# Kernel optimization log

Hardware: AMD Instinct MI355X
Metric: run time of the kernel (lower is better)

## Reference

```python
import jax, jax.numpy as jnp
import numpy as np

N = 50000      # nodes
E = 800000     # edges (avg degree 16)
D_IN = 128
D_H = 128
D_OUT = 8


def setup_inputs() -> dict:
    key = jax.random.key(0)
    ks = jax.random.split(key, 12)
    def lin(k, fan_in, shape):
        return (jax.random.normal(k, shape, jnp.float32) / np.float32(np.sqrt(fan_in)))
    return {
        "node_features": jax.random.normal(ks[0], (N, D_IN), jnp.float32),
        "edge_index": jax.random.randint(ks[1], (2, E), 0, N, jnp.int32),
        # 3 GCNConv layers: weight [in, out] + bias [out]
        "W0": lin(ks[2], D_IN, (D_IN, D_H)), "b0": jnp.zeros((D_H,), jnp.float32),
        "W1": lin(ks[3], D_H, (D_H, D_H)),  "b1": jnp.zeros((D_H,), jnp.float32),
        "W2": lin(ks[4], D_H, (D_H, D_H)),  "b2": jnp.zeros((D_H,), jnp.float32),
        # classifier MLP: hidden -> hidden//2 -> output
        "cW1": lin(ks[5], D_H, (D_H, D_H // 2)), "cb1": jnp.zeros((D_H // 2,), jnp.float32),
        "cW2": lin(ks[6], D_H // 2, (D_H // 2, D_OUT)), "cb2": jnp.zeros((D_OUT,), jnp.float32),
    }


def _gcn_norm(edge_index, n):
    # PyG GCNConv default: add self-loops, symmetric D^-1/2 (A+I) D^-1/2 normalization
    loops = jnp.arange(n, dtype=edge_index.dtype)
    src = jnp.concatenate([edge_index[0], loops])   # message sources j
    dst = jnp.concatenate([edge_index[1], loops])   # aggregation targets i
    deg = jax.ops.segment_sum(jnp.ones_like(src, dtype=jnp.float32), dst, num_segments=n)
    dinv = jax.lax.rsqrt(jnp.maximum(deg, 1.0))     # deg >= 1 due to self-loops
    norm = dinv[src] * dinv[dst]                    # [E+N]
    return src, dst, norm


def _gcn_conv(x, W, b, src, dst, norm, n):
    h = x @ W                                        # [N, out] dense transform first (PyG order)
    msg = h[src] * norm[:, None]                     # gather + scale  [E+N, out]
    out = jax.ops.segment_sum(msg, dst, num_segments=n)  # scatter-add
    return out + b


def reference(node_features, edge_index, W0, b0, W1, b1, W2, b2, cW1, cb1, cW2, cb2):
    n = node_features.shape[0]
    src, dst, norm = _gcn_norm(edge_index, n)
    x = jax.nn.relu(_gcn_conv(node_features, W0, b0, src, dst, norm, n))  # dropout is identity in eval
    x = jax.nn.relu(_gcn_conv(x, W1, b1, src, dst, norm, n))
    x = _gcn_conv(x, W2, b2, src, dst, norm, n)       # last conv: no relu/dropout
    # classifier MLP (dropout identity in eval)
    h = jax.nn.relu(x @ cW1 + cb1)
    return h @ cW2 + cb2                              # [N, D_OUT]
```

## Files before the change

kernel.cpp:

```cpp
#include <hip/hip_runtime.h>
#include <hip/hip_fp16.h>


#define CAP 48
#define FPG 512

using half8v  = __attribute__((ext_vector_type(8))) _Float16;
using float4v = __attribute__((ext_vector_type(4))) float;

__global__ __launch_bounds__(256) void fill_kernel(const int* __restrict__ src,
                                                   const int* __restrict__ dst, int e, int n,
                                                   const float* __restrict__ W0,
                                                   const float* __restrict__ W1,
                                                   const float* __restrict__ W2,
                                                   const float* __restrict__ cW1,
                                                   const float* __restrict__ cb1,
                                                   const float* __restrict__ b2,
                                                   int* __restrict__ cnt,
                                                   unsigned short* __restrict__ col,
                                                   __half* __restrict__ Wf0,
                                                   __half* __restrict__ Wf1,
                                                   __half* __restrict__ Wfc,
                                                   float* __restrict__ bc) {
    int b = blockIdx.x;
    int tid = threadIdx.x;
    const int FILLB = 4 * FPG;
    if (b < FILLB) {
        int g = b & 3;
        int cb = b >> 2;
        int npp = (n + 3) >> 2;
        int lo = g * npp;
        int hi = min(lo + npp, n);
        int step = FPG * 256;
        int base = cb * 256 + tid;
        int dv[7], sv[7];
        #pragma unroll
        for (int k = 0; k < 7; k++) {
            int i = base + k * step;
            if (i < e) {
                dv[k] = __builtin_nontemporal_load(dst + i);
                sv[k] = __builtin_nontemporal_load(src + i);
            }
        }
        #pragma unroll
        for (int k = 0; k < 7; k++) {
            int i = base + k * step;
            if (i < e) {
                int d = dv[k];
                if (d >= lo && d < hi) {
                    int c = atomicAdd(&cnt[d], 1);
                    if (c < CAP) col[d * CAP + c] = (unsigned short)sv[k];
                }
            }
        }
        return;
    }
    b -= FILLB;
    if (b < 16) {
        int t = b * 256 + tid;
        const float* W = (t < 2048) ? W0 : W1;
        __half* Wf = (t < 2048) ? Wf0 : Wf1;
        int u = t & 2047;
        int lane = u & 63, tile = (u >> 6) & 7, kk = u >> 9;
        int k0 = kk * 32 + (lane >> 4) * 8;
        int nn = tile * 16 + (lane & 15);
        __half tmp[8];
        #pragma unroll
        for (int j = 0; j < 8; j++) tmp[j] = __float2half(W[(k0 + j) * 128 + nn]);
        *(float4*)(Wf + (size_t)u * 8) = *(const float4*)tmp;
        return;
    }
    b -= 16;
    if (b < 4) {
        int u = b * 256 + tid;
        int lane = u & 63, tile = (u >> 6) & 3, kk = u >> 8;
        int k0 = kk * 32 + (lane >> 4) * 8;
        int nn = tile * 16 + (lane & 15);
        float a[8] = {};
        for (int m = 0; m < 128; m++) {
            float c = cW1[m * 64 + nn];
            #pragma unroll
            for (int j = 0; j < 8; j++) a[j] = fmaf(W2[(k0 + j) * 128 + m], c, a[j]);
        }
        __half tmp[8];
        #pragma unroll
        for (int j = 0; j < 8; j++) tmp[j] = __float2half(a[j]);
        *(float4*)(Wfc + (size_t)u * 8) = *(const float4*)tmp;
        return;
    }
    if (tid < 64) {
        float a = cb1[tid];
        for (int k = 0; k < 128; k++) a = fmaf(b2[k], cW1[k * 64 + tid], a);
        bc[tid] = a;
    }
}

__global__ __launch_bounds__(256) void gemm0_mfma(const float* __restrict__ x,
                                                  const __half* __restrict__ Wf,
                                                  const int* __restrict__ cnt,
                                                  __half* __restrict__ out, int n) {
    int tid = threadIdx.x;
    int wv = tid >> 6, lane = tid & 63;
    int row0 = blockIdx.x * 64 + wv * 16;
    int m = lane & 15, q = lane >> 4;
    int ra = min(row0 + m, n - 1);
    const float* xrow = x + (size_t)ra * 128 + q * 8;
    const _Float16* wf = (const _Float16*)Wf + (size_t)lane * 8;
    float4v acc[8] = {};
    #pragma unroll
    for (int kk = 0; kk < 4; kk++) {
        float4 xa = *(const float4*)(xrow + kk * 32);
        float4 xb = *(const float4*)(xrow + kk * 32 + 4);
        half8v a;
        a[0] = (_Float16)xa.x; a[1] = (_Float16)xa.y;
        a[2] = (_Float16)xa.z; a[3] = (_Float16)xa.w;
        a[4] = (_Float16)xb.x; a[5] = (_Float16)xb.y;
        a[6] = (_Float16)xb.z; a[7] = (_Float16)xb.w;
        #pragma unroll
        for (int t8 = 0; t8 < 8; t8++) {
            half8v bfr = *(const half8v*)(wf + (size_t)(kk * 8 + t8) * 512);
            acc[t8] = __builtin_amdgcn_mfma_f32_16x16x32_f16(a, bfr, acc[t8], 0, 0, 0);
        }
    }
    int rowv[4];
    float dr[4];
    #pragma unroll
    for (int r = 0; r < 4; r++) {
        rowv[r] = row0 + q * 4 + r;
        dr[r] = (rowv[r] < n) ? rsqrtf((float)(cnt[rowv[r]] + 1)) : 0.f;
    }
    #pragma unroll
    for (int t8 = 0; t8 < 8; t8++) {
        #pragma unroll
        for (int r = 0; r < 4; r++) {
            if (rowv[r] < n)
                out[(size_t)(t8 >> 1) * n * 32 + (size_t)rowv[r] * 32 + (t8 & 1) * 16 + m] =
                    __float2half(acc[t8][r] * dr[r]);
        }
    }
}

__global__ __launch_bounds__(256) void gemm_mfma(const __half* __restrict__ x,
                                                 const __half* __restrict__ Wf,
                                                 const int* __restrict__ cnt,
                                                 __half* __restrict__ out, int n) {
    int tid = threadIdx.x;
    int wv = tid >> 6, lane = tid & 63;
    int row0 = blockIdx.x * 64 + wv * 16;
    int m = lane & 15, q = lane >> 4;
    int ra = min(row0 + m, n - 1);
    const _Float16* xb = (const _Float16*)x;
    const _Float16* wf = (const _Float16*)Wf + (size_t)lane * 8;
    float4v acc[8] = {};
    #pragma unroll
    for (int kk = 0; kk < 4; kk++) {
        int tki = kk * 2 + (q >> 1);
        half8v a = *(const half8v*)(xb + (size_t)(tki >> 1) * n * 32 + (size_t)ra * 32 +
                                    (tki & 1) * 16 + (q & 1) * 8);
        #pragma unroll
        for (int t8 = 0; t8 < 8; t8++) {
            half8v bfr = *(const half8v*)(wf + (size_t)(kk * 8 + t8) * 512);
            acc[t8] = __builtin_amdgcn_mfma_f32_16x16x32_f16(a, bfr, acc[t8], 0, 0, 0);
        }
    }
    int rowv[4];
    float dr[4];
    #pragma unroll
    for (int r = 0; r < 4; r++) {
        rowv[r] = row0 + q * 4 + r;
        dr[r] = (rowv[r] < n) ? rsqrtf((float)(cnt[rowv[r]] + 1)) : 0.f;
    }
    #pragma unroll
    for (int t8 = 0; t8 < 8; t8++) {
        #pragma unroll
        for (int r = 0; r < 4; r++) {
            if (rowv[r] < n)
                out[(size_t)(t8 >> 1) * n * 32 + (size_t)rowv[r] * 32 + (t8 & 1) * 16 + m] =
                    __float2half(acc[t8][r] * dr[r]);
        }
    }
}

__global__ __launch_bounds__(256) void gemm_t_mfma(const __half* __restrict__ x,
                                                   const __half* __restrict__ Wf,
                                                   __half* __restrict__ out, int n) {
    int tid = threadIdx.x;
    int wv = tid >> 6, lane = tid & 63;
    int row0 = blockIdx.x * 64 + wv * 16;
    int m = lane & 15, q = lane >> 4;
    int ra = min(row0 + m, n - 1);
    const _Float16* xb = (const _Float16*)x;
    const _Float16* wf = (const _Float16*)Wf + (size_t)lane * 8;
    float4v acc[4] = {};
    #pragma unroll
    for (int kk = 0; kk < 4; kk++) {
        int tki = kk * 2 + (q >> 1);
        half8v a = *(const half8v*)(xb + (size_t)(tki >> 1) * n * 32 + (size_t)ra * 32 +
                                    (tki & 1) * 16 + (q & 1) * 8);
        #pragma unroll
        for (int t8 = 0; t8 < 4; t8++) {
            half8v bfr = *(const half8v*)(wf + (size_t)(kk * 4 + t8) * 512);
            acc[t8] = __builtin_amdgcn_mfma_f32_16x16x32_f16(a, bfr, acc[t8], 0, 0, 0);
        }
    }
    int rowv[4];
    #pragma unroll
    for (int r = 0; r < 4; r++) rowv[r] = row0 + q * 4 + r;
    #pragma unroll
    for (int t8 = 0; t8 < 4; t8++) {
        #pragma unroll
        for (int r = 0; r < 4; r++) {
            if (rowv[r] < n)
                out[(size_t)(t8 >> 1) * n * 32 + (size_t)rowv[r] * 32 + (t8 & 1) * 16 + m] =
                    __float2half(acc[t8][r]);
        }
    }
}

__global__ __launch_bounds__(256) void agg_tiled(const __half* __restrict__ hin,
                                                 const int* __restrict__ cnt,
                                                 const unsigned short* __restrict__ col,
                                                 const float* __restrict__ bias,
                                                 __half* __restrict__ hout,
                                                 int n, float one, int relu,
                                                 int scale_out, int ftsh) {
    int ft = blockIdx.x & ((1 << ftsh) - 1);
    int nb = blockIdx.x >> ftsh;
    int tid = threadIdx.x;
    int node = nb * 64 + (tid >> 2);
    int q = tid & 3;
    int ic = min(node, n - 1);
    const _Float16* hsl = (const _Float16*)hin + (size_t)ft * n * 32 + q * 8;
    int ci = cnt[ic];
    int len = min(ci, CAP);
    float di = rsqrtf((float)(ci + 1));
    half8v s = *(const half8v*)(hsl + (size_t)ic * 32);
    float acc[8];
    #pragma unroll
    for (int t = 0; t < 8; t++) acc[t] = (float)s[t];
    const unsigned short* crow = col + ic * CAP;
    int nfull = len >> 4;
    for (int f = 0; f < nfull; f++) {
        int k0 = f * 16;
        uint4 ca = *(const uint4*)(crow + k0);
        uint4 cb = *(const uint4*)(crow + k0 + 8);
        int j[16];
        j[0]  = ca.x & 0xffff; j[1]  = ca.x >> 16;
        j[2]  = ca.y & 0xffff; j[3]  = ca.y >> 16;
        j[4]  = ca.z & 0xffff; j[5]  = ca.z >> 16;
        j[6]  = ca.w & 0xffff; j[7]  = ca.w >> 16;
        j[8]  = cb.x & 0xffff; j[9]  = cb.x >> 16;
        j[10] = cb.y & 0xffff; j[11] = cb.y >> 16;
        j[12] = cb.z & 0xffff; j[13] = cb.z >> 16;
        j[14] = cb.w & 0xffff; j[15] = cb.w >> 16;
        half8v v[16];
        #pragma unroll
        for (int u = 0; u < 16; u++) v[u] = *(const half8v*)(hsl + (size_t)j[u] * 32);
        #pragma unroll
        for (int u = 0; u < 16; u++) {
            #pragma unroll
            for (int t = 0; t < 8; t++) acc[t] = fmaf((float)v[u][t], one, acc[t]);
        }
    }
    int k0 = nfull * 16;
    if (k0 < len) {
        int rem = len - k0;
        uint4 ca = *(const uint4*)(crow + k0);
        uint4 cb = *(const uint4*)(crow + k0 + 8);
        int j[16];
        j[0]  = ca.x & 0xffff; j[1]  = ca.x >> 16;
        j[2]  = ca.y & 0xffff; j[3]  = ca.y >> 16;
        j[4]  = ca.z & 0xffff; j[5]  = ca.z >> 16;
        j[6]  = ca.w & 0xffff; j[7]  = ca.w >> 16;
        j[8]  = cb.x & 0xffff; j[9]  = cb.x >> 16;
        j[10] = cb.y & 0xffff; j[11] = cb.y >> 16;
        j[12] = cb.z & 0xffff; j[13] = cb.z >> 16;
        j[14] = cb.w & 0xffff; j[15] = cb.w >> 16;
        float w[16];
        half8v v[16];
        #pragma unroll
        for (int u = 0; u < 16; u++) {
            bool val = u < rem;
            w[u] = val ? one : 0.f;
            int jj = val ? j[u] : ic;
            v[u] = *(const half8v*)(hsl + (size_t)jj * 32);
        }
        #pragma unroll
        for (int u = 0; u < 16; u++) {
            #pragma unroll
            for (int t = 0; t < 8; t++) acc[t] = fmaf((float)v[u][t], w[u], acc[t]);
        }
    }
    if (node < n) {
        float post = scale_out ? di : 1.f;
        half8v o;
        #pragma unroll
        for (int t = 0; t < 8; t++) {
            float bv = bias ? bias[ft * 32 + q * 8 + t] : 0.f;
            float a = fmaf(acc[t], di, bv);
            if (relu) a = fmaxf(a, 0.f);
            o[t] = (_Float16)(a * post);
        }
        *(half8v*)((_Float16*)hout + (size_t)ft * n * 32 + (size_t)node * 32 + q * 8) = o;
    }
}

__global__ __launch_bounds__(256) void cls_kernel(const __half* __restrict__ h,
                                                  const float* __restrict__ cW2,
                                                  const float* __restrict__ cb2,
                                                  float* __restrict__ out, int n) {
    __shared__ _Float16 hs[64][72];
    int tid = threadIdx.x;
    int node0 = blockIdx.x * 64;
    int nl = tid >> 2, q = tid & 3;
    int ic = min(node0 + nl, n - 1);
    #pragma unroll
    for (int ft = 0; ft < 2; ft++) {
        half8v v = *(const half8v*)((const _Float16*)h + (size_t)ft * n * 32 +
                                    (size_t)ic * 32 + q * 8);
        *(half8v*)&hs[nl][ft * 32 + q * 8] = v;
    }
    __syncthreads();
    #pragma unroll
    for (int p = 0; p < 2; p++) {
        int idx = p * 256 + tid;
        int rl = idx >> 3, c2 = idx & 7;
        int row = node0 + rl;
        if (row < n) {
            float a = cb2[c2];
            #pragma unroll 8
            for (int k = 0; k < 64; k++) a = fmaf((float)hs[rl][k], cW2[k * 8 + c2], a);
            out[row * 8 + c2] = a;
        }
    }
}

extern "C" void kernel_launch(void* const* d_in, const int* in_sizes, int n_in,
                              void* d_out, int out_size, void* d_ws, size_t ws_size,
                              hipStream_t stream) {
    const float* x   = (const float*)d_in[0];
    const int*   ei  = (const int*)d_in[1];
    const float* W0  = (const float*)d_in[2];
    const float* b0  = (const float*)d_in[3];
    const float* W1  = (const float*)d_in[4];
    const float* b1  = (const float*)d_in[5];
    const float* W2  = (const float*)d_in[6];
    const float* b2  = (const float*)d_in[7];
    const float* cW1 = (const float*)d_in[8];
    const float* cb1 = (const float*)d_in[9];
    const float* cW2 = (const float*)d_in[10];
    const float* cb2 = (const float*)d_in[11];
    float* out = (float*)d_out;

    int N = in_sizes[0] / 128;
    int E = in_sizes[1] / 2;
    const int* src = ei;
    const int* dst = ei + E;

    char* ws = (char*)d_ws;
    size_t off = 0;
    auto alloc = [&](size_t bytes) {
        void* p = ws + off;
        off = (off + bytes + 255) & ~(size_t)255;
        return p;
    };
    int* cnt              = (int*)alloc((size_t)N * 4);
    unsigned short* col   = (unsigned short*)alloc((size_t)N * CAP * 2);
    __half* Wf0           = (__half*)alloc((size_t)128 * 128 * 2);
    __half* Wf1           = (__half*)alloc((size_t)128 * 128 * 2);
    __half* Wfc           = (__half*)alloc((size_t)128 * 64 * 2);
    float* bc             = (float*)alloc(64 * 4);
    __half* hA            = (__half*)alloc((size_t)N * 128 * 2);
    __half* hB            = (__half*)alloc((size_t)N * 128 * 2);

    hipMemsetAsync(cnt, 0, (size_t)N * 4, stream);

    fill_kernel<<<4 * FPG + 21, 256, 0, stream>>>(src, dst, E, N, W0, W1, W2,
                                                  cW1, cb1, b2,
                                                  cnt, col, Wf0, Wf1, Wfc, bc);

    int NBLK = (N + 63) / 64;
    gemm0_mfma<<<NBLK, 256, 0, stream>>>(x, Wf0, cnt, hA, N);
    agg_tiled<<<NBLK * 4, 256, 0, stream>>>(hA, cnt, col, b0, hB, N, 1.0f, 1, 0, 2);
    gemm_mfma<<<NBLK, 256, 0, stream>>>(hB, Wf1, cnt, hA, N);
    agg_tiled<<<NBLK * 4, 256, 0, stream>>>(hA, cnt, col, b1, hB, N, 1.0f, 1, 1, 2);
    gemm_t_mfma<<<NBLK, 256, 0, stream>>>(hB, Wfc, hA, N);
    agg_tiled<<<NBLK * 2, 256, 0, stream>>>(hA, cnt, col, bc, hB, N, 1.0f, 1, 0, 1);
    cls_kernel<<<NBLK, 256, 0, stream>>>(hB, cW2, cb2, out, N);
}
```

Before: 245.9 us.

## Fuse all GCN stages into one cooperative persistent kernel with grid syncs

Replaces the memset and the seven separate kernel launches with a single cooperative persistent kernel. It zeroes the counts, builds the CSR, preps the weights, then runs the gemm, aggregation and classifier phases, separated by grid-wide syncs. Each phase loops over the same virtual blocks as before. This removes launch gaps and the memset, at the cost of grid barrier overhead, a grid capped at 1024 blocks, and possible register pressure from one fused kernel.

```diff
diff --git a/kernel.cpp b/kernel.cpp
--- a/kernel.cpp
+++ b/kernel.cpp
@@ -1,390 +1,417 @@
 #include <hip/hip_runtime.h>
 #include <hip/hip_fp16.h>
+#include <hip/hip_cooperative_groups.h>
+
+namespace cg = cooperative_groups;
 
 
 #define CAP 48
-#define FPG 512
 
 using half8v  = __attribute__((ext_vector_type(8))) _Float16;
 using float4v = __attribute__((ext_vector_type(4))) float;
 
-__global__ __launch_bounds__(256) void fill_kernel(const int* __restrict__ src,
-                                                   const int* __restrict__ dst, int e, int n,
-                                                   const float* __restrict__ W0,
-                                                   const float* __restrict__ W1,
-                                                   const float* __restrict__ W2,
-                                                   const float* __restrict__ cW1,
-                                                   const float* __restrict__ cb1,
-                                                   const float* __restrict__ b2,
-                                                   int* __restrict__ cnt,
-                                                   unsigned short* __restrict__ col,
-                                                   __half* __restrict__ Wf0,
-                                                   __half* __restrict__ Wf1,
-                                                   __half* __restrict__ Wfc,
-                                                   float* __restrict__ bc) {
-    int b = blockIdx.x;
-    int tid = threadIdx.x;
-    const int FILLB = 4 * FPG;
-    if (b < FILLB) {
-        int g = b & 3;
-        int cb = b >> 2;
-        int npp = (n + 3) >> 2;
-        int lo = g * npp;
-        int hi = min(lo + npp, n);
-        int step = FPG * 256;
-        int base = cb * 256 + tid;
-        int dv[7], sv[7];
-        #pragma unroll
-        for (int k = 0; k < 7; k++) {
-            int i = base + k * step;
-            if (i < e) {
-                dv[k] = __builtin_nontemporal_load(dst + i);
-                sv[k] = __builtin_nontemporal_load(src + i);
-            }
-        }
-        #pragma unroll
-        for (int k = 0; k < 7; k++) {
-            int i = base + k * step;
-            if (i < e) {
-                int d = dv[k];
-                if (d >= lo && d < hi) {
-                    int c = atomicAdd(&cnt[d], 1);
-                    if (c < CAP) col[d * CAP + c] = (unsigned short)sv[k];
-                }
-            }
-        }
-        return;
-    }
-    b -= FILLB;
-    if (b < 16) {
-        int t = b * 256 + tid;
-        const float* W = (t < 2048) ? W0 : W1;
-        __half* Wf = (t < 2048) ? Wf0 : Wf1;
-        int u = t & 2047;
-        int lane = u & 63, tile = (u >> 6) & 7, kk = u >> 9;
-        int k0 = kk * 32 + (lane >> 4) * 8;
-        int nn = tile * 16 + (lane & 15);
-        __half tmp[8];
-        #pragma unroll
-        for (int j = 0; j < 8; j++) tmp[j] = __float2half(W[(k0 + j) * 128 + nn]);
-        *(float4*)(Wf + (size_t)u * 8) = *(const float4*)tmp;
-        return;
-    }
-    b -= 16;
-    if (b < 4) {
-        int u = b * 256 + tid;
-        int lane = u & 63, tile = (u >> 6) & 3, kk = u >> 8;
-        int k0 = kk * 32 + (lane >> 4) * 8;
-        int nn = tile * 16 + (lane & 15);
-        float a[8] = {};
-        for (int m = 0; m < 128; m++) {
-            float c = cW1[m * 64 + nn];
-            #pragma unroll
-            for (int j = 0; j < 8; j++) a[j] = fmaf(W2[(k0 + j) * 128 + m], c, a[j]);
-        }
-        __half tmp[8];
-        #pragma unroll
-        for (int j = 0; j < 8; j++) tmp[j] = __float2half(a[j]);
-        *(float4*)(Wfc + (size_t)u * 8) = *(const float4*)tmp;
-        return;
-    }
+struct MegaArgs {
+  const int* src; const int* dst;
+  const float* x;
+  const float* W0; const float* b0;
+  const float* W1; const float* b1;
+  const float* W2; const float* b2;
+  const float* cW1; const float* cb1;
+  const float* cW2; const float* cb2;
+  int* cnt; unsigned short* col;
+  __half* Wf0; __half* Wf1; __half* Wfc; float* bc;
+  __half* hA; __half* hB; float* out;
+  int e; int n; int nblk;
+  float one;
+};
+
+__device__ __forceinline__ void fill_vb(int vb, int tid, const MegaArgs& A) {
+  int g = vb & 3;
+  int cb = vb >> 2;
+  int npp = (A.n + 3) >> 2;
+  int lo = g * npp;
+  int hi = min(lo + npp, A.n);
+  const int step = 512 * 256;
+  int base = cb * 256 + tid;
+  int dv[7], sv[7];
+  #pragma unroll
+  for (int k = 0; k < 7; k++) {
+    int i = base + k * step;
+    if (i < A.e) {
+      dv[k] = __builtin_nontemporal_load(A.dst + i);
+      sv[k] = __builtin_nontemporal_load(A.src + i);
+    }
+  }
+  #pragma unroll
+  for (int k = 0; k < 7; k++) {
+    int i = base + k * step;
+    if (i < A.e) {
+      int d = dv[k];
+      if (d >= lo && d < hi) {
+        int c = atomicAdd(&A.cnt[d], 1);
+        if (c < CAP) A.col[d * CAP + c] = (unsigned short)sv[k];
+      }
+    }
+  }
+  for (int i = base + 7 * step; i < A.e; i += step) {
+    int d = __builtin_nontemporal_load(A.dst + i);
+    int s = __builtin_nontemporal_load(A.src + i);
+    if (d >= lo && d < hi) {
+      int c = atomicAdd(&A.cnt[d], 1);
+      if (c < CAP) A.col[d * CAP + c] = (unsigned short)s;
+    }
+  }
+}
+
+__device__ __forceinline__ void wprep_vb(int b, int tid, const MegaArgs& A) {
+  if (b < 16) {
+    int t = b * 256 + tid;
+    const float* W = (t < 2048) ? A.W0 : A.W1;
+    __half* Wf = (t < 2048) ? A.Wf0 : A.Wf1;
+    int u = t & 2047;
+    int lane = u & 63, tile = (u >> 6) & 7, kk = u >> 9;
+    int k0 = kk * 32 + (lane >> 4) * 8;
+    int nn = tile * 16 + (lane & 15);
+    __half tmp[8];
+    #pragma unroll
+    for (int j = 0; j < 8; j++) tmp[j] = __float2half(W[(k0 + j) * 128 + nn]);
+    *(float4*)(Wf + (size_t)u * 8) = *(const float4*)tmp;
+  } else if (b < 20) {
+    int u = (b - 16) * 256 + tid;
+    int lane = u & 63, tile = (u >> 6) & 3, kk = u >> 8;
+    int k0 = kk * 32 + (lane >> 4) * 8;
+    int nn = tile * 16 + (lane & 15);
+    float a[8] = {};
+    for (int m = 0; m < 128; m++) {
+      float c = A.cW1[m * 64 + nn];
+      #pragma unroll
+      for (int j = 0; j < 8; j++) a[j] = fmaf(A.W2[(k0 + j) * 128 + m], c, a[j]);
+    }
+    __half tmp[8];
+    #pragma unroll
+    for (int j = 0; j < 8; j++) tmp[j] = __float2half(a[j]);
+    *(float4*)(A.Wfc + (size_t)u * 8) = *(const float4*)tmp;
+  } else {
     if (tid < 64) {
-        float a = cb1[tid];
-        for (int k = 0; k < 128; k++) a = fmaf(b2[k], cW1[k * 64 + tid], a);
-        bc[tid] = a;
-    }
-}
-
-__global__ __launch_bounds__(256) void gemm0_mfma(const float* __restrict__ x,
-                                                  const __half* __restrict__ Wf,
-                                                  const int* __restrict__ cnt,
-                                                  __half* __restrict__ out, int n) {
-    int tid = threadIdx.x;
-    int wv = tid >> 6, lane = tid & 63;
-    int row0 = blockIdx.x * 64 + wv * 16;
-    int m = lane & 15, q = lane >> 4;
-    int ra = min(row0 + m, n - 1);
-    const float* xrow = x + (size_t)ra * 128 + q * 8;
-    const _Float16* wf = (const _Float16*)Wf + (size_t)lane * 8;
-    float4v acc[8] = {};
-    #pragma unroll
-    for (int kk = 0; kk < 4; kk++) {
-        float4 xa = *(const float4*)(xrow + kk * 32);
-        float4 xb = *(const float4*)(xrow + kk * 32 + 4);
-        half8v a;
-        a[0] = (_Float16)xa.x; a[1] = (_Float16)xa.y;
-        a[2] = (_Float16)xa.z; a[3] = (_Float16)xa.w;
-        a[4] = (_Float16)xb.x; a[5] = (_Float16)xb.y;
-        a[6] = (_Float16)xb.z; a[7] = (_Float16)xb.w;
-        #pragma unroll
-        for (int t8 = 0; t8 < 8; t8++) {
-            half8v bfr = *(const half8v*)(wf + (size_t)(kk * 8 + t8) * 512);
-            acc[t8] = __builtin_amdgcn_mfma_f32_16x16x32_f16(a, bfr, acc[t8], 0, 0, 0);
-        }
-    }
-    int rowv[4];
-    float dr[4];
+      float a = A.cb1[tid];
+      for (int k = 0; k < 128; k++) a = fmaf(A.b2[k], A.cW1[k * 64 + tid], a);
+      A.bc[tid] = a;
+    }
+  }
+}
+
+__device__ __forceinline__ void gemm0_vb(int vb, int tid, const MegaArgs& A) {
+  int wv = tid >> 6, lane = tid & 63;
+  int row0 = vb * 64 + wv * 16;
+  int m = lane & 15, q = lane >> 4;
+  int ra = min(row0 + m, A.n - 1);
+  const float* xrow = A.x + (size_t)ra * 128 + q * 8;
+  const _Float16* wf = (const _Float16*)A.Wf0 + (size_t)lane * 8;
+  float4v acc[8] = {};
+  #pragma unroll
+  for (int kk = 0; kk < 4; kk++) {
+    float4 xa = *(const float4*)(xrow + kk * 32);
+    float4 xb = *(const float4*)(xrow + kk * 32 + 4);
+    half8v a;
+    a[0] = (_Float16)xa.x; a[1] = (_Float16)xa.y;
+    a[2] = (_Float16)xa.z; a[3] = (_Float16)xa.w;
+    a[4] = (_Float16)xb.x; a[5] = (_Float16)xb.y;
+    a[6] = (_Float16)xb.z; a[7] = (_Float16)xb.w;
+    #pragma unroll
+    for (int t8 = 0; t8 < 8; t8++) {
+      half8v bfr = *(const half8v*)(wf + (size_t)(kk * 8 + t8) * 512);
+      acc[t8] = __builtin_amdgcn_mfma_f32_16x16x32_f16(a, bfr, acc[t8], 0, 0, 0);
+    }
+  }
+  int rowv[4];
+  float dr[4];
+  #pragma unroll
+  for (int r = 0; r < 4; r++) {
+    rowv[r] = row0 + q * 4 + r;
+    dr[r] = (rowv[r] < A.n) ? rsqrtf((float)(A.cnt[rowv[r]] + 1)) : 0.f;
+  }
+  #pragma unroll
+  for (int t8 = 0; t8 < 8; t8++) {
     #pragma unroll
     for (int r = 0; r < 4; r++) {
-        rowv[r] = row0 + q * 4 + r;
-        dr[r] = (rowv[r] < n) ? rsqrtf((float)(cnt[rowv[r]] + 1)) : 0.f;
-    }
+      if (rowv[r] < A.n)
+        A.hA[(size_t)(t8 >> 1) * A.n * 32 + (size_t)rowv[r] * 32 + (t8 & 1) * 16 + m] =
+            __float2half(acc[t8][r] * dr[r]);
+    }
+  }
+}
+
+__device__ __forceinline__ void gemm_vb(int vb, int tid, const __half* xin,
+                                        const __half* Wf, const int* cnt,
+                                        __half* outp, int n) {
+  int wv = tid >> 6, lane = tid & 63;
+  int row0 = vb * 64 + wv * 16;
+  int m = lane & 15, q = lane >> 4;
+  int ra = min(row0 + m, n - 1);
+  const _Float16* xb = (const _Float16*)xin;
+  const _Float16* wf = (const _Float16*)Wf + (size_t)lane * 8;
+  float4v acc[8] = {};
+  #pragma unroll
+  for (int kk = 0; kk < 4; kk++) {
+    int tki = kk * 2 + (q >> 1);
+    half8v a = *(const half8v*)(xb + (size_t)(tki >> 1) * n * 32 + (size_t)ra * 32 +
+                                (tki & 1) * 16 + (q & 1) * 8);
     #pragma unroll
     for (int t8 = 0; t8 < 8; t8++) {
-        #pragma unroll
-        for (int r = 0; r < 4; r++) {
-            if (rowv[r] < n)
-                out[(size_t)(t8 >> 1) * n * 32 + (size_t)rowv[r] * 32 + (t8 & 1) * 16 + m] =
-                    __float2half(acc[t8][r] * dr[r]);
-        }
-    }
-}
-
-__global__ __launch_bounds__(256) void gemm_mfma(const __half* __restrict__ x,
-                                                 const __half* __restrict__ Wf,
-                                                 const int* __restrict__ cnt,
-                                                 __half* __restrict__ out, int n) {
-    int tid = threadIdx.x;
-    int wv = tid >> 6, lane = tid & 63;
-    int row0 = blockIdx.x * 64 + wv * 16;
-    int m = lane & 15, q = lane >> 4;
-    int ra = min(row0 + m, n - 1);
-    const _Float16* xb = (const _Float16*)x;
-    const _Float16* wf = (const _Float16*)Wf + (size_t)lane * 8;
-    float4v acc[8] = {};
-    #pragma unroll
-    for (int kk = 0; kk < 4; kk++) {
-        int tki = kk * 2 + (q >> 1);
-        half8v a = *(const half8v*)(xb + (size_t)(tki >> 1) * n * 32 + (size_t)ra * 32 +
-                                    (tki & 1) * 16 + (q & 1) * 8);
-        #pragma unroll
-        for (int t8 = 0; t8 < 8; t8++) {
-            half8v bfr = *(const half8v*)(wf + (size_t)(kk * 8 + t8) * 512);
-            acc[t8] = __builtin_amdgcn_mfma_f32_16x16x32_f16(a, bfr, acc[t8], 0, 0, 0);
-        }
-    }
-    int rowv[4];
-    float dr[4];
+      half8v bfr = *(const half8v*)(wf + (size_t)(kk * 8 + t8) * 512);
+      acc[t8] = __builtin_amdgcn_mfma_f32_16x16x32_f16(a, bfr, acc[t8], 0, 0, 0);
+    }
+  }
+  int rowv[4];
+  float dr[4];
+  #pragma unroll
+  for (int r = 0; r < 4; r++) {
+    rowv[r] = row0 + q * 4 + r;
+    dr[r] = (rowv[r] < n) ? rsqrtf((float)(cnt[rowv[r]] + 1)) : 0.f;
+  }
+  #pragma unroll
+  for (int t8 = 0; t8 < 8; t8++) {
     #pragma unroll
     for (int r = 0; r < 4; r++) {
-        rowv[r] = row0 + q * 4 + r;
-        dr[r] = (rowv[r] < n) ? rsqrtf((float)(cnt[rowv[r]] + 1)) : 0.f;
-    }
-    #pragma unroll
-    for (int t8 = 0; t8 < 8; t8++) {
-        #pragma unroll
-        for (int r = 0; r < 4; r++) {
-            if (rowv[r] < n)
-                out[(size_t)(t8 >> 1) * n * 32 + (size_t)rowv[r] * 32 + (t8 & 1) * 16 + m] =
-                    __float2half(acc[t8][r] * dr[r]);
-        }
-    }
-}
-
-__global__ __launch_bounds__(256) void gemm_t_mfma(const __half* __restrict__ x,
-                                                   const __half* __restrict__ Wf,
-                                                   __half* __restrict__ out, int n) {
-    int tid = threadIdx.x;
-    int wv = tid >> 6, lane = tid & 63;
-    int row0 = blockIdx.x * 64 + wv * 16;
-    int m = lane & 15, q = lane >> 4;
-    int ra = min(row0 + m, n - 1);
-    const _Float16* xb = (const _Float16*)x;
-    const _Float16* wf = (const _Float16*)Wf + (size_t)lane * 8;
-    float4v acc[4] = {};
-    #pragma unroll
-    for (int kk = 0; kk < 4; kk++) {
-        int tki = kk * 2 + (q >> 1);
-        half8v a = *(const half8v*)(xb + (size_t)(tki >> 1) * n * 32 + (size_t)ra * 32 +
-                                    (tki & 1) * 16 + (q & 1) * 8);
-        #pragma unroll
-        for (int t8 = 0; t8 < 4; t8++) {
-            half8v bfr = *(const half8v*)(wf + (size_t)(kk * 4 + t8) * 512);
-            acc[t8] = __builtin_amdgcn_mfma_f32_16x16x32_f16(a, bfr, acc[t8], 0, 0, 0);
-        }
-    }
-    int rowv[4];
-    #pragma unroll
-    for (int r = 0; r < 4; r++) rowv[r] = row0 + q * 4 + r;
+      if (rowv[r] < n)
+        outp[(size_t)(t8 >> 1) * n * 32 + (size_t)rowv[r] * 32 + (t8 & 1) * 16 + m] =
+            __float2half(acc[t8][r] * dr[r]);
+    }
+  }
+}
+
+__device__ __forceinline__ void gemmt_vb(int vb, int tid, const __half* xin,
+                                         const __half* Wf, __half* outp, int n) {
+  int wv = tid >> 6, lane = tid & 63;
+  int row0 = vb * 64 + wv * 16;
+  int m = lane & 15, q = lane >> 4;
+  int ra = min(row0 + m, n - 1);
+  const _Float16* xb = (const _Float16*)xin;
+  const _Float16* wf = (const _Float16*)Wf + (size_t)lane * 8;
+  float4v acc[4] = {};
+  #pragma unroll
+  for (int kk = 0; kk < 4; kk++) {
+    int tki = kk * 2 + (q >> 1);
+    half8v a = *(const half8v*)(xb + (size_t)(tki >> 1) * n * 32 + (size_t)ra * 32 +
+                                (tki & 1) * 16 + (q & 1) * 8);
     #pragma unroll
     for (int t8 = 0; t8 < 4; t8++) {
-        #pragma unroll
-        for (int r = 0; r < 4; r++) {
-            if (rowv[r] < n)
-                out[(size_t)(t8 >> 1) * n * 32 + (size_t)rowv[r] * 32 + (t8 & 1) * 16 + m] =
-                    __float2half(acc[t8][r]);
-        }
-    }
-}
-
-__global__ __launch_bounds__(256) void agg_tiled(const __half* __restrict__ hin,
-                                                 const int* __restrict__ cnt,
-                                                 const unsigned short* __restrict__ col,
-                                                 const float* __restrict__ bias,
-                                                 __half* __restrict__ hout,
-                                                 int n, float one, int relu,
-                                                 int scale_out, int ftsh) {
-    int ft = blockIdx.x & ((1 << ftsh) - 1);
-    int nb = blockIdx.x >> ftsh;
-    int tid = threadIdx.x;
-    int node = nb * 64 + (tid >> 2);
-    int q = tid & 3;
-    int ic = min(node, n - 1);
-    const _Float16* hsl = (const _Float16*)hin + (size_t)ft * n * 32 + q * 8;
-    int ci = cnt[ic];
-    int len = min(ci, CAP);
-    float di = rsqrtf((float)(ci + 1));
-    half8v s = *(const half8v*)(hsl + (size_t)ic * 32);
-    float acc[8];
-    #pragma unroll
-    for (int t = 0; t < 8; t++) acc[t] = (float)s[t];
-    const unsigned short* crow = col + ic * CAP;
-    int nfull = len >> 4;
-    for (int f = 0; f < nfull; f++) {
-        int k0 = f * 16;
-        uint4 ca = *(const uint4*)(crow + k0);
-        uint4 cb = *(const uint4*)(crow + k0 + 8);
-        int j[16];
-        j[0]  = ca.x & 0xffff; j[1]  = ca.x >> 16;
-        j[2]  = ca.y & 0xffff; j[3]  = ca.y >> 16;
-        j[4]  = ca.z & 0xffff; j[5]  = ca.z >> 16;
-        j[6]  = ca.w & 0xffff; j[7]  = ca.w >> 16;
-        j[8]  = cb.x & 0xffff; j[9]  = cb.x >> 16;
-        j[10] = cb.y & 0xffff; j[11] = cb.y >> 16;
-        j[12] = cb.z & 0xffff; j[13] = cb.z >> 16;
-        j[14] = cb.w & 0xffff; j[15] = cb.w >> 16;
-        half8v v[16];
-        #pragma unroll
-        for (int u = 0; u < 16; u++) v[u] = *(const half8v*)(hsl + (size_t)j[u] * 32);
-        #pragma unroll
-        for (int u = 0; u < 16; u++) {
-            #pragma unroll
-            for (int t = 0; t < 8; t++) acc[t] = fmaf((float)v[u][t], one, acc[t]);
-        }
-    }
-    int k0 = nfull * 16;
-    if (k0 < len) {
-        int rem = len - k0;
-        uint4 ca = *(const uint4*)(crow + k0);
-        uint4 cb = *(const uint4*)(crow + k0 + 8);
-        int j[16];
-        j[0]  = ca.x & 0xffff; j[1]  = ca.x >> 16;
-        j[2]  = ca.y & 0xffff; j[3]  = ca.y >> 16;
-        j[4]  = ca.z & 0xffff; j[5]  = ca.z >> 16;
-        j[6]  = ca.w & 0xffff; j[7]  = ca.w >> 16;
-        j[8]  = cb.x & 0xffff; j[9]  = cb.x >> 16;
-        j[10] = cb.y & 0xffff; j[11] = cb.y >> 16;
-        j[12] = cb.z & 0xffff; j[13] = cb.z >> 16;
-        j[14] = cb.w & 0xffff; j[15] = cb.w >> 16;
-        float w[16];
-        half8v v[16];
-        #pragma unroll
-        for (int u = 0; u < 16; u++) {
-            bool val = u < rem;
-            w[u] = val ? one : 0.f;
-            int jj = val ? j[u] : ic;
-            v[u] = *(const half8v*)(hsl + (size_t)jj * 32);
-        }
-        #pragma unroll
-        for (int u = 0; u < 16; u++) {
-            #pragma unroll
-            for (int t = 0; t < 8; t++) acc[t] = fmaf((float)v[u][t], w[u], acc[t]);
-        }
-    }
-    if (node < n) {
-        float post = scale_out ? di : 1.f;
-        half8v o;
-        #pragma unroll
-        for (int t = 0; t < 8; t++) {
-            float bv = bias ? bias[ft * 32 + q * 8 + t] : 0.f;
-            float a = fmaf(acc[t], di, bv);
-            if (relu) a = fmaxf(a, 0.f);
-            o[t] = (_Float16)(a * post);
-        }
-        *(half8v*)((_Float16*)hout + (size_t)ft * n * 32 + (size_t)node * 32 + q * 8) = o;
-    }
-}
-
-__global__ __launch_bounds__(256) void cls_kernel(const __half* __restrict__ h,
-                                                  const float* __restrict__ cW2,
-                                                  const float* __restrict__ cb2,
-                                                  float* __restrict__ out, int n) {
-    __shared__ _Float16 hs[64][72];
-    int tid = threadIdx.x;
-    int node0 = blockIdx.x * 64;
+      half8v bfr = *(const half8v*)(wf + (size_t)(kk * 4 + t8) * 512);
+      acc[t8] = __builtin_amdgcn_mfma_f32_16x16x32_f16(a, bfr, acc[t8], 0, 0, 0);
+    }
+  }
+  int rowv[4];
+  #pragma unroll
+  for (int r = 0; r < 4; r++) rowv[r] = row0 + q * 4 + r;
+  #pragma unroll
+  for (int t8 = 0; t8 < 4; t8++) {
+    #pragma unroll
+    for (int r = 0; r < 4; r++) {
+      if (rowv[r] < n)
+        outp[(size_t)(t8 >> 1) * n * 32 + (size_t)rowv[r] * 32 + (t8 & 1) * 16 + m] =
+            __float2half(acc[t8][r]);
+    }
+  }
+}
+
+__device__ __forceinline__ void agg_vb(int vb, int tid, const __half* hin,
+                                       const int* cnt, const unsigned short* col,
+                                       const float* bias, __half* hout, int n,
+                                       float one, int relu, int scale_out, int ftsh) {
+  int ft = vb & ((1 << ftsh) - 1);
+  int nb = vb >> ftsh;
+  int node = nb * 64 + (tid >> 2);
+  int q = tid & 3;
+  int ic = min(node, n - 1);
+  const _Float16* hsl = (const _Float16*)hin + (size_t)ft * n * 32 + q * 8;
+  int ci = cnt[ic];
+  int len = min(ci, CAP);
+  float di = rsqrtf((float)(ci + 1));
+  half8v s = *(const half8v*)(hsl + (size_t)ic * 32);
+  float acc[8];
+  #pragma unroll
+  for (int t = 0; t < 8; t++) acc[t] = (float)s[t];
+  const unsigned short* crow = col + ic * CAP;
+  int nfull = len >> 4;
+  for (int f = 0; f < nfull; f++) {
+    int k0 = f * 16;
+    uint4 ca = *(const uint4*)(crow + k0);
+    uint4 cb = *(const uint4*)(crow + k0 + 8);
+    int j[16];
+    j[0]  = ca.x & 0xffff; j[1]  = ca.x >> 16;
+    j[2]  = ca.y & 0xffff; j[3]  = ca.y >> 16;
+    j[4]  = ca.z & 0xffff; j[5]  = ca.z >> 16;
+    j[6]  = ca.w & 0xffff; j[7]  = ca.w >> 16;
+    j[8]  = cb.x & 0xffff; j[9]  = cb.x >> 16;
+    j[10] = cb.y & 0xffff; j[11] = cb.y >> 16;
+    j[12] = cb.z & 0xffff; j[13] = cb.z >> 16;
+    j[14] = cb.w & 0xffff; j[15] = cb.w >> 16;
+    half8v v[16];
+    #pragma unroll
+    for (int u = 0; u < 16; u++) v[u] = *(const half8v*)(hsl + (size_t)j[u] * 32);
+    #pragma unroll
+    for (int u = 0; u < 16; u++) {
+      #pragma unroll
+      for (int t = 0; t < 8; t++) acc[t] = fmaf((float)v[u][t], one, acc[t]);
+    }
+  }
+  int k0 = nfull * 16;
+  if (k0 < len) {
+    int rem = len - k0;
+    uint4 ca = *(const uint4*)(crow + k0);
+    uint4 cb = *(const uint4*)(crow + k0 + 8);
+    int j[16];
+    j[0]  = ca.x & 0xffff; j[1]  = ca.x >> 16;
+    j[2]  = ca.y & 0xffff; j[3]  = ca.y >> 16;
+    j[4]  = ca.z & 0xffff; j[5]  = ca.z >> 16;
+    j[6]  = ca.w & 0xffff; j[7]  = ca.w >> 16;
+    j[8]  = cb.x & 0xffff; j[9]  = cb.x >> 16;
+    j[10] = cb.y & 0xffff; j[11] = cb.y >> 16;
+    j[12] = cb.z & 0xffff; j[13] = cb.z >> 16;
+    j[14] = cb.w & 0xffff; j[15] = cb.w >> 16;
+    float w[16];
+    half8v v[16];
+    #pragma unroll
+    for (int u = 0; u < 16; u++) {
+      bool val = u < rem;
+      w[u] = val ? one : 0.f;
+      int jj = val ? j[u] : ic;
+      v[u] = *(const half8v*)(hsl + (size_t)jj * 32);
+    }
+    #pragma unroll
+    for (int u = 0; u < 16; u++) {
+      #pragma unroll
+      for (int t = 0; t < 8; t++) acc[t] = fmaf((float)v[u][t], w[u], acc[t]);
+    }
+  }
+  if (node < n) {
+    float post = scale_out ? di : 1.f;
+    half8v o;
+    #pragma unroll
+    for (int t = 0; t < 8; t++) {
+      float bv = bias ? bias[ft * 32 + q * 8 + t] : 0.f;
+      float a = fmaf(acc[t], di, bv);
+      if (relu) a = fmaxf(a, 0.f);
+      o[t] = (_Float16)(a * post);
+    }
+    *(half8v*)((_Float16*)hout + (size_t)ft * n * 32 + (size_t)node * 32 + q * 8) = o;
+  }
+}
+
+__global__ __launch_bounds__(256, 4) void mega(MegaArgs A) {
+  cg::grid_group gg = cg::this_grid();
+  int tid = threadIdx.x;
+  int bid = blockIdx.x;
+  int G = gridDim.x;
+  __shared__ _Float16 hs[64][72];
+
+  for (int i = bid * 256 + tid; i < A.n; i += G * 256) A.cnt[i] = 0;
+  gg.sync();
+
+  for (int vb = bid; vb < 2048 + 21; vb += G) {
+    if (vb < 2048) fill_vb(vb, tid, A);
+    else wprep_vb(vb - 2048, tid, A);
+  }
+  gg.sync();
+
+  for (int vb = bid; vb < A.nblk; vb += G) gemm0_vb(vb, tid, A);
+  gg.sync();
+
+  for (int vb = bid; vb < A.nblk * 4; vb += G)
+    agg_vb(vb, tid, A.hA, A.cnt, A.col, A.b0, A.hB, A.n, A.one, 1, 0, 2);
+  gg.sync();
+
+  for (int vb = bid; vb < A.nblk; vb += G)
+    gemm_vb(vb, tid, A.hB, A.Wf1, A.cnt, A.hA, A.n);
+  gg.sync();
+
+  for (int vb = bid; vb < A.nblk * 4; vb += G)
+    agg_vb(vb, tid, A.hA, A.cnt, A.col, A.b1, A.hB, A.n, A.one, 1, 1, 2);
+  gg.sync();
+
+  for (int vb = bid; vb < A.nblk; vb += G)
+    gemmt_vb(vb, tid, A.hB, A.Wfc, A.hA, A.n);
+  gg.sync();
+
+  for (int vb = bid; vb < A.nblk * 2; vb += G)
+    agg_vb(vb, tid, A.hA, A.cnt, A.col, A.bc, A.hB, A.n, A.one, 1, 0, 1);
+  gg.sync();
+
+  for (int vb = bid; vb < A.nblk; vb += G) {
+    int node0 = vb * 64;
     int nl = tid >> 2, q = tid & 3;
-    int ic = min(node0 + nl, n - 1);
+    int ic = min(node0 + nl, A.n - 1);
     #pragma unroll
     for (int ft = 0; ft < 2; ft++) {
-        half8v v = *(const half8v*)((const _Float16*)h + (size_t)ft * n * 32 +
-                                    (size_t)ic * 32 + q * 8);
-        *(half8v*)&hs[nl][ft * 32 + q * 8] = v;
+      half8v v = *(const half8v*)((const _Float16*)A.hB + (size_t)ft * A.n * 32 +
+                                  (size_t)ic * 32 + q * 8);
+      *(half8v*)&hs[nl][ft * 32 + q * 8] = v;
     }
     __syncthreads();
     #pragma unroll
     for (int p = 0; p < 2; p++) {
-        int idx = p * 256 + tid;
-        int rl = idx >> 3, c2 = idx & 7;
-        int row = node0 + rl;
-        if (row < n) {
-            float a = cb2[c2];
-            #pragma unroll 8
-            for (int k = 0; k < 64; k++) a = fmaf((float)hs[rl][k], cW2[k * 8 + c2], a);
-            out[row * 8 + c2] = a;
-        }
-    }
+      int idx = p * 256 + tid;
+      int rl = idx >> 3, c2 = idx & 7;
+      int row = node0 + rl;
+      if (row < A.n) {
+        float a = A.cb2[c2];
+        #pragma unroll 8
+        for (int k = 0; k < 64; k++)
+          a = fmaf((float)hs[rl][k], A.cW2[k * 8 + c2], a);
+        A.out[row * 8 + c2] = a;
+      }
+    }
+    __syncthreads();
+  }
 }
 
 extern "C" void kernel_launch(void* const* d_in, const int* in_sizes, int n_in,
                               void* d_out, int out_size, void* d_ws, size_t ws_size,
                               hipStream_t stream) {
-    const float* x   = (const float*)d_in[0];
-    const int*   ei  = (const int*)d_in[1];
-    const float* W0  = (const float*)d_in[2];
-    const float* b0  = (const float*)d_in[3];
-    const float* W1  = (const float*)d_in[4];
-    const float* b1  = (const float*)d_in[5];
-    const float* W2  = (const float*)d_in[6];
-    const float* b2  = (const float*)d_in[7];
-    const float* cW1 = (const float*)d_in[8];
-    const float* cb1 = (const float*)d_in[9];
-    const float* cW2 = (const float*)d_in[10];
-    const float* cb2 = (const float*)d_in[11];
-    float* out = (float*)d_out;
-
-    int N = in_sizes[0] / 128;
-    int E = in_sizes[1] / 2;
-    const int* src = ei;
-    const int* dst = ei + E;
-
-    char* ws = (char*)d_ws;
-    size_t off = 0;
-    auto alloc = [&](size_t bytes) {
-        void* p = ws + off;
-        off = (off + bytes + 255) & ~(size_t)255;
-        return p;
-    };
-    int* cnt              = (int*)alloc((size_t)N * 4);
-    unsigned short* col   = (unsigned short*)alloc((size_t)N * CAP * 2);
-    __half* Wf0           = (__half*)alloc((size_t)128 * 128 * 2);
-    __half* Wf1           = (__half*)alloc((size_t)128 * 128 * 2);
-    __half* Wfc           = (__half*)alloc((size_t)128 * 64 * 2);
-    float* bc             = (float*)alloc(64 * 4);
-    __half* hA            = (__half*)alloc((size_t)N * 128 * 2);
-    __half* hB            = (__half*)alloc((size_t)N * 128 * 2);
-
-    hipMemsetAsync(cnt, 0, (size_t)N * 4, stream);
-
-    fill_kernel<<<4 * FPG + 21, 256, 0, stream>>>(src, dst, E, N, W0, W1, W2,
-                                                  cW1, cb1, b2,
-                                                  cnt, col, Wf0, Wf1, Wfc, bc);
-
-    int NBLK = (N + 63) / 64;
-    gemm0_mfma<<<NBLK, 256, 0, stream>>>(x, Wf0, cnt, hA, N);
-    agg_tiled<<<NBLK * 4, 256, 0, stream>>>(hA, cnt, col, b0, hB, N, 1.0f, 1, 0, 2);
-    gemm_mfma<<<NBLK, 256, 0, stream>>>(hB, Wf1, cnt, hA, N);
-    agg_tiled<<<NBLK * 4, 256, 0, stream>>>(hA, cnt, col, b1, hB, N, 1.0f, 1, 1, 2);
-    gemm_t_mfma<<<NBLK, 256, 0, stream>>>(hB, Wfc, hA, N);
-    agg_tiled<<<NBLK * 2, 256, 0, stream>>>(hA, cnt, col, bc, hB, N, 1.0f, 1, 0, 1);
-    cls_kernel<<<NBLK, 256, 0, stream>>>(hB, cW2, cb2, out, N);
-}
+  MegaArgs A;
+  A.x   = (const float*)d_in[0];
+  const int* ei = (const int*)d_in[1];
+  A.W0  = (const float*)d_in[2];
+  A.b0  = (const float*)d_in[3];
+  A.W1  = (const float*)d_in[4];
+  A.b1  = (const float*)d_in[5];
+  A.W2  = (const float*)d_in[6];
+  A.b2  = (const float*)d_in[7];
+  A.cW1 = (const float*)d_in[8];
+  A.cb1 = (const float*)d_in[9];
+  A.cW2 = (const float*)d_in[10];
+  A.cb2 = (const float*)d_in[11];
+  A.out = (float*)d_out;
+
+  A.n = in_sizes[0] / 128;
+  A.e = in_sizes[1] / 2;
+  A.src = ei;
+  A.dst = ei + A.e;
+  A.nblk = (A.n + 63) / 64;
+  A.one = 1.0f;
+
+  char* ws = (char*)d_ws;
+  size_t off = 0;
+  auto alloc = [&](size_t bytes) {
+    void* p = ws + off;
+    off = (off + bytes + 255) & ~(size_t)255;
+    return p;
+  };
+  A.cnt = (int*)alloc((size_t)A.n * 4);
+  A.col = (unsigned short*)alloc((size_t)A.n * CAP * 2);
+  A.Wf0 = (__half*)alloc((size_t)128 * 128 * 2);
+  A.Wf1 = (__half*)alloc((size_t)128 * 128 * 2);
+  A.Wfc = (__half*)alloc((size_t)128 * 64 * 2);
+  A.bc  = (float*)alloc(64 * 4);
+  A.hA  = (__half*)alloc((size_t)A.n * 128 * 2);
+  A.hB  = (__half*)alloc((size_t)A.n * 128 * 2);
+
+  int maxb = 0;
+  hipError_t oe = hipOccupancyMaxActiveBlocksPerMultiprocessor(&maxb, mega, 256, 0);
+  if (oe != hipSuccess || maxb < 1) maxb = 4;
+  int grid = maxb * 256;
+  if (grid > 1024) grid = 1024;
+
+  void* params[] = { &A };
+  hipLaunchCooperativeKernel(mega, dim3(grid), dim3(256), params, 0, stream);
+}
```

Measured after the change: 796.8 us. 224% more time.

## Merge edge fill with first-layer GEMM and defer degree scaling to separate pass

Applied to the files above, without the earlier changes.

The edge bucketing and weight-prep blocks now share one launch with the layer-0 GEMM, which builds its fp16 W0 fragments in LDS per block instead of reading a prepacked buffer. Because the degrees are not final while that GEMM runs, its output is written unscaled in fp32 to a new buffer, and a separate scale kernel converts it to fp16 with the D^-1/2 factor. The goal is to overlap the atomic-heavy fill with GEMM compute and drop one dependent launch, at the cost of an extra fp32 write and read of N×128 values plus an additional kernel. The aggregation tail also gains a cheaper 8-wide path when 8 or fewer neighbours remain, and the fill grid is doubled with a strided loop over leftover edges.

```diff
diff --git a/kernel.cpp b/kernel.cpp
--- a/kernel.cpp
+++ b/kernel.cpp
@@ -3,141 +3,160 @@
 
 
 #define CAP 48
-#define FPG 512
+#define FPG 1024
 
 using half8v  = __attribute__((ext_vector_type(8))) _Float16;
 using float4v = __attribute__((ext_vector_type(4))) float;
 
-__global__ __launch_bounds__(256) void fill_kernel(const int* __restrict__ src,
-                                                   const int* __restrict__ dst, int e, int n,
-                                                   const float* __restrict__ W0,
-                                                   const float* __restrict__ W1,
-                                                   const float* __restrict__ W2,
-                                                   const float* __restrict__ cW1,
-                                                   const float* __restrict__ cb1,
-                                                   const float* __restrict__ b2,
-                                                   int* __restrict__ cnt,
-                                                   unsigned short* __restrict__ col,
-                                                   __half* __restrict__ Wf0,
-                                                   __half* __restrict__ Wf1,
-                                                   __half* __restrict__ Wfc,
-                                                   float* __restrict__ bc) {
-    int b = blockIdx.x;
-    int tid = threadIdx.x;
-    const int FILLB = 4 * FPG;
-    if (b < FILLB) {
-        int g = b & 3;
-        int cb = b >> 2;
-        int npp = (n + 3) >> 2;
-        int lo = g * npp;
-        int hi = min(lo + npp, n);
-        int step = FPG * 256;
-        int base = cb * 256 + tid;
-        int dv[7], sv[7];
-        #pragma unroll
-        for (int k = 0; k < 7; k++) {
-            int i = base + k * step;
-            if (i < e) {
-                dv[k] = __builtin_nontemporal_load(dst + i);
-                sv[k] = __builtin_nontemporal_load(src + i);
-            }
-        }
-        #pragma unroll
-        for (int k = 0; k < 7; k++) {
-            int i = base + k * step;
-            if (i < e) {
-                int d = dv[k];
-                if (d >= lo && d < hi) {
-                    int c = atomicAdd(&cnt[d], 1);
-                    if (c < CAP) col[d * CAP + c] = (unsigned short)sv[k];
-                }
-            }
-        }
-        return;
-    }
-    b -= FILLB;
-    if (b < 16) {
-        int t = b * 256 + tid;
-        const float* W = (t < 2048) ? W0 : W1;
-        __half* Wf = (t < 2048) ? Wf0 : Wf1;
-        int u = t & 2047;
-        int lane = u & 63, tile = (u >> 6) & 7, kk = u >> 9;
-        int k0 = kk * 32 + (lane >> 4) * 8;
-        int nn = tile * 16 + (lane & 15);
-        __half tmp[8];
-        #pragma unroll
-        for (int j = 0; j < 8; j++) tmp[j] = __float2half(W[(k0 + j) * 128 + nn]);
-        *(float4*)(Wf + (size_t)u * 8) = *(const float4*)tmp;
-        return;
-    }
-    b -= 16;
-    if (b < 4) {
-        int u = b * 256 + tid;
-        int lane = u & 63, tile = (u >> 6) & 3, kk = u >> 8;
-        int k0 = kk * 32 + (lane >> 4) * 8;
-        int nn = tile * 16 + (lane & 15);
-        float a[8] = {};
-        for (int m = 0; m < 128; m++) {
-            float c = cW1[m * 64 + nn];
-            #pragma unroll
-            for (int j = 0; j < 8; j++) a[j] = fmaf(W2[(k0 + j) * 128 + m], c, a[j]);
-        }
-        __half tmp[8];
-        #pragma unroll
-        for (int j = 0; j < 8; j++) tmp[j] = __float2half(a[j]);
-        *(float4*)(Wfc + (size_t)u * 8) = *(const float4*)tmp;
-        return;
-    }
-    if (tid < 64) {
+__global__ __launch_bounds__(256) void merged_kernel(
+    const int* __restrict__ src, const int* __restrict__ dst, int e, int n,
+    int nblk, const float* __restrict__ x,
+    const float* __restrict__ W0, const float* __restrict__ W1,
+    const float* __restrict__ W2, const float* __restrict__ cW1,
+    const float* __restrict__ cb1, const float* __restrict__ b2,
+    int* __restrict__ cnt, unsigned short* __restrict__ col,
+    __half* __restrict__ Wf1, __half* __restrict__ Wfc,
+    float* __restrict__ bc, float* __restrict__ hF) {
+  int b = blockIdx.x;
+  int tid = threadIdx.x;
+  const int FILLB = 4 * FPG;
+  if (b < FILLB) {
+    int g = b & 3;
+    int cb = b >> 2;
+    int npp = (n + 3) >> 2;
+    int lo = g * npp;
+    int hi = min(lo + npp, n);
+    const int step = FPG * 256;
+    int base = cb * 256 + tid;
+    int dv[4], sv[4];
+    #pragma unroll
+    for (int k = 0; k < 4; k++) {
+      int i = base + k * step;
+      if (i < e) {
+        dv[k] = __builtin_nontemporal_load(dst + i);
+        sv[k] = __builtin_nontemporal_load(src + i);
+      }
+    }
+    #pragma unroll
+    for (int k = 0; k < 4; k++) {
+      int i = base + k * step;
+      if (i < e) {
+        int d = dv[k];
+        if (d >= lo && d < hi) {
+          int c = atomicAdd(&cnt[d], 1);
+          if (c < CAP) col[d * CAP + c] = (unsigned short)sv[k];
+        }
+      }
+    }
+    for (int i = base + 4 * step; i < e; i += step) {
+      int d = __builtin_nontemporal_load(dst + i);
+      int s = __builtin_nontemporal_load(src + i);
+      if (d >= lo && d < hi) {
+        int c = atomicAdd(&cnt[d], 1);
+        if (c < CAP) col[d * CAP + c] = (unsigned short)s;
+      }
+    }
+    return;
+  }
+  b -= FILLB;
+  if (b < 13) {
+    if (b < 8) {
+      int t = b * 256 + tid;
+      int lane = t & 63, tile = (t >> 6) & 7, kk = t >> 9;
+      int k0 = kk * 32 + (lane >> 4) * 8;
+      int nn = tile * 16 + (lane & 15);
+      __half tmp[8];
+      #pragma unroll
+      for (int j = 0; j < 8; j++) tmp[j] = __float2half(W1[(k0 + j) * 128 + nn]);
+      *(float4*)(Wf1 + (size_t)t * 8) = *(const float4*)tmp;
+    } else if (b < 12) {
+      int u = (b - 8) * 256 + tid;
+      int lane = u & 63, tile = (u >> 6) & 3, kk = u >> 8;
+      int k0 = kk * 32 + (lane >> 4) * 8;
+      int nn = tile * 16 + (lane & 15);
+      float a[8] = {};
+      for (int m = 0; m < 128; m++) {
+        float c = cW1[m * 64 + nn];
+        #pragma unroll
+        for (int j = 0; j < 8; j++) a[j] = fmaf(W2[(k0 + j) * 128 + m], c, a[j]);
+      }
+      __half tmp[8];
+      #pragma unroll
+      for (int j = 0; j < 8; j++) tmp[j] = __float2half(a[j]);
+      *(float4*)(Wfc + (size_t)u * 8) = *(const float4*)tmp;
+    } else {
+      if (tid < 64) {
         float a = cb1[tid];
         for (int k = 0; k < 128; k++) a = fmaf(b2[k], cW1[k * 64 + tid], a);
         bc[tid] = a;
-    }
-}
-
-__global__ __launch_bounds__(256) void gemm0_mfma(const float* __restrict__ x,
-                                                  const __half* __restrict__ Wf,
-                                                  const int* __restrict__ cnt,
-                                                  __half* __restrict__ out, int n) {
-    int tid = threadIdx.x;
-    int wv = tid >> 6, lane = tid & 63;
-    int row0 = blockIdx.x * 64 + wv * 16;
-    int m = lane & 15, q = lane >> 4;
-    int ra = min(row0 + m, n - 1);
-    const float* xrow = x + (size_t)ra * 128 + q * 8;
-    const _Float16* wf = (const _Float16*)Wf + (size_t)lane * 8;
-    float4v acc[8] = {};
-    #pragma unroll
-    for (int kk = 0; kk < 4; kk++) {
-        float4 xa = *(const float4*)(xrow + kk * 32);
-        float4 xb = *(const float4*)(xrow + kk * 32 + 4);
-        half8v a;
-        a[0] = (_Float16)xa.x; a[1] = (_Float16)xa.y;
-        a[2] = (_Float16)xa.z; a[3] = (_Float16)xa.w;
-        a[4] = (_Float16)xb.x; a[5] = (_Float16)xb.y;
-        a[6] = (_Float16)xb.z; a[7] = (_Float16)xb.w;
-        #pragma unroll
-        for (int t8 = 0; t8 < 8; t8++) {
-            half8v bfr = *(const half8v*)(wf + (size_t)(kk * 8 + t8) * 512);
-            acc[t8] = __builtin_amdgcn_mfma_f32_16x16x32_f16(a, bfr, acc[t8], 0, 0, 0);
-        }
-    }
-    int rowv[4];
-    float dr[4];
+      }
+    }
+    return;
+  }
+  int vb = b - 13;
+  __shared__ _Float16 wlds[128 * 128];
+  for (int u = tid; u < 2048; u += 256) {
+    int lane = u & 63, tile = (u >> 6) & 7, kk = u >> 9;
+    int k0 = kk * 32 + (lane >> 4) * 8;
+    int nn = tile * 16 + (lane & 15);
+    _Float16 tmp[8];
+    #pragma unroll
+    for (int j = 0; j < 8; j++) tmp[j] = (_Float16)W0[(k0 + j) * 128 + nn];
+    *(half8v*)(wlds + (size_t)u * 8) = *(const half8v*)tmp;
+  }
+  __syncthreads();
+  int wv = tid >> 6, lane = tid & 63;
+  int row0 = vb * 64 + wv * 16;
+  int m = lane & 15, q = lane >> 4;
+  int ra = min(row0 + m, n - 1);
+  const float* xrow = x + (size_t)ra * 128 + q * 8;
+  float4v acc[8] = {};
+  #pragma unroll
+  for (int kk = 0; kk < 4; kk++) {
+    float4 xa = *(const float4*)(xrow + kk * 32);
+    float4 xb = *(const float4*)(xrow + kk * 32 + 4);
+    half8v a;
+    a[0] = (_Float16)xa.x; a[1] = (_Float16)xa.y;
+    a[2] = (_Float16)xa.z; a[3] = (_Float16)xa.w;
+    a[4] = (_Float16)xb.x; a[5] = (_Float16)xb.y;
+    a[6] = (_Float16)xb.z; a[7] = (_Float16)xb.w;
+    #pragma unroll
+    for (int t8 = 0; t8 < 8; t8++) {
+      half8v bfr = *(const half8v*)(wlds + (size_t)(kk * 8 + t8) * 512 + lane * 8);
+      acc[t8] = __builtin_amdgcn_mfma_f32_16x16x32_f16(a, bfr, acc[t8], 0, 0, 0);
+    }
+  }
+  int rowv[4];
+  #pragma unroll
+  for (int r = 0; r < 4; r++) rowv[r] = row0 + q * 4 + r;
+  #pragma unroll
+  for (int t8 = 0; t8 < 8; t8++) {
     #pragma unroll
     for (int r = 0; r < 4; r++) {
-        rowv[r] = row0 + q * 4 + r;
-        dr[r] = (rowv[r] < n) ? rsqrtf((float)(cnt[rowv[r]] + 1)) : 0.f;
-    }
-    #pragma unroll
-    for (int t8 = 0; t8 < 8; t8++) {
-        #pragma unroll
-        for (int r = 0; r < 4; r++) {
-            if (rowv[r] < n)
-                out[(size_t)(t8 >> 1) * n * 32 + (size_t)rowv[r] * 32 + (t8 & 1) * 16 + m] =
-                    __float2half(acc[t8][r] * dr[r]);
-        }
-    }
+      if (rowv[r] < n)
+        hF[(size_t)(t8 >> 1) * n * 32 + (size_t)rowv[r] * 32 + (t8 & 1) * 16 + m] =
+            acc[t8][r];
+    }
+  }
+}
+
+__global__ __launch_bounds__(256) void scale_kernel(const float* __restrict__ hF,
+                                                    const int* __restrict__ cnt,
+                                                    __half* __restrict__ hA, int n) {
+  int gid = blockIdx.x * 256 + threadIdx.x;
+  int total = n * 16;
+  if (gid < total) {
+    int q = gid & 3;
+    int r = gid >> 2;
+    int nd = r % n;
+    size_t off = (size_t)r * 32 + q * 8;
+    float di = rsqrtf((float)(cnt[nd] + 1));
+    const float* s = hF + off;
+    half8v o;
+    #pragma unroll
+    for (int t = 0; t < 8; t++) o[t] = (_Float16)(s[t] * di);
+    *(half8v*)((_Float16*)hA + off) = o;
+  }
 }
 
 __global__ __launch_bounds__(256) void gemm_mfma(const __half* __restrict__ x,
@@ -263,8 +282,8 @@
         }
     }
     int k0 = nfull * 16;
-    if (k0 < len) {
-        int rem = len - k0;
+    int rem = len - k0;
+    if (rem > 8) {
         uint4 ca = *(const uint4*)(crow + k0);
         uint4 cb = *(const uint4*)(crow + k0 + 8);
         int j[16];
@@ -290,6 +309,27 @@
             #pragma unroll
             for (int t = 0; t < 8; t++) acc[t] = fmaf((float)v[u][t], w[u], acc[t]);
         }
+    } else if (rem > 0) {
+        uint4 ca = *(const uint4*)(crow + k0);
+        int j[8];
+        j[0] = ca.x & 0xffff; j[1] = ca.x >> 16;
+        j[2] = ca.y & 0xffff; j[3] = ca.y >> 16;
+        j[4] = ca.z & 0xffff; j[5] = ca.z >> 16;
+        j[6] = ca.w & 0xffff; j[7] = ca.w >> 16;
+        float w[8];
+        half8v v[8];
+        #pragma unroll
+        for (int u = 0; u < 8; u++) {
+            bool val = u < rem;
+            w[u] = val ? one : 0.f;
+            int jj = val ? j[u] : ic;
+            v[u] = *(const half8v*)(hsl + (size_t)jj * 32);
+        }
+        #pragma unroll
+        for (int u = 0; u < 8; u++) {
+            #pragma unroll
+            for (int t = 0; t < 8; t++) acc[t] = fmaf((float)v[u][t], w[u], acc[t]);
+        }
     }
     if (node < n) {
         float post = scale_out ? di : 1.f;
@@ -328,8 +368,9 @@
         int row = node0 + rl;
         if (row < n) {
             float a = cb2[c2];
+            const _Float16* hr = &hs[rl][0];
             #pragma unroll 8
-            for (int k = 0; k < 64; k++) a = fmaf((float)hs[rl][k], cW2[k * 8 + c2], a);
+            for (int k = 0; k < 64; k++) a = fmaf((float)hr[k], cW2[k * 8 + c2], a);
             out[row * 8 + c2] = a;
         }
     }
@@ -366,21 +407,21 @@
     };
     int* cnt              = (int*)alloc((size_t)N * 4);
     unsigned short* col   = (unsigned short*)alloc((size_t)N * CAP * 2);
-    __half* Wf0           = (__half*)alloc((size_t)128 * 128 * 2);
     __half* Wf1           = (__half*)alloc((size_t)128 * 128 * 2);
     __half* Wfc           = (__half*)alloc((size_t)128 * 64 * 2);
     float* bc             = (float*)alloc(64 * 4);
     __half* hA            = (__half*)alloc((size_t)N * 128 * 2);
     __half* hB            = (__half*)alloc((size_t)N * 128 * 2);
+    float* hF             = (float*)alloc((size_t)N * 128 * 4);
 
     hipMemsetAsync(cnt, 0, (size_t)N * 4, stream);
 
-    fill_kernel<<<4 * FPG + 21, 256, 0, stream>>>(src, dst, E, N, W0, W1, W2,
-                                                  cW1, cb1, b2,
-                                                  cnt, col, Wf0, Wf1, Wfc, bc);
-
     int NBLK = (N + 63) / 64;
-    gemm0_mfma<<<NBLK, 256, 0, stream>>>(x, Wf0, cnt, hA, N);
+    merged_kernel<<<4 * FPG + 13 + NBLK, 256, 0, stream>>>(
+        src, dst, E, N, NBLK, x, W0, W1, W2, cW1, cb1, b2,
+        cnt, col, Wf1, Wfc, bc, hF);
+    scale_kernel<<<(N * 16 + 255) / 256, 256, 0, stream>>>(hF, cnt, hA, N);
+
     agg_tiled<<<NBLK * 4, 256, 0, stream>>>(hA, cnt, col, b0, hB, N, 1.0f, 1, 0, 2);
     gemm_mfma<<<NBLK, 256, 0, stream>>>(hB, Wf1, cnt, hA, N);
     agg_tiled<<<NBLK * 4, 256, 0, stream>>>(hA, cnt, col, b1, hB, N, 1.0f, 1, 1, 2);
```

Result: slower. 253.8 us (+3.2%).
